# Kernel optimization log

Measured on AMD Instinct MI355X. Metric: run time of the kernel, lower is better.

The kernel has to match this reference:

```python
import jax, jax.numpy as jnp
import numpy as np
import math

N_HEADS = 16  # matches init_kwargs n_heads


def setup_inputs() -> dict:
    key = jax.random.key(0)
    k1, k2, k3 = jax.random.split(key, 3)
    B, S, D = 8, 1024, 1024
    x = jax.random.normal(k1, (B, S, D), dtype=jnp.float32)
    Wc = jax.random.normal(k2, (D, 3 * D), dtype=jnp.float32) * 0.02
    bc = jnp.zeros((3 * D,), dtype=jnp.float32)
    Wo = jax.random.normal(k3, (D, D), dtype=jnp.float32) * 0.02
    bo = jnp.zeros((D,), dtype=jnp.float32)
    return {"x": x, "Wc": Wc, "bc": bc, "Wo": Wo, "bo": bo}


def reference(x, Wc, bc, Wo, bo):
    B, S, D = x.shape
    H = N_HEADS
    hd = D // H
    qkv = x @ Wc + bc                         # [B,S,3D]
    q, k, v = jnp.split(qkv, 3, axis=2)
    q = q.reshape(B, S, H, hd)
    k = k.reshape(B, S, H, hd)
    v = v.reshape(B, S, H, hd)
    # NOTE: source scales by sqrt(d_size), not sqrt(head_dim)
    scores = jnp.einsum("bqhd,bkhd->bhqk", q, k) / math.sqrt(D)
    # source mask: triu(ones) kept, zeros (k < q) filled with float32 min
    # i.e. attend only to positions k >= q (anti-causal, faithful to source)
    keep = jnp.triu(jnp.ones((S, S), dtype=bool))  # [S,S]
    neg = jnp.finfo(jnp.float32).min
    scores = jnp.where(keep[None, None, :, :], scores, neg)
    attn = jax.nn.softmax(scores, axis=-1)    # [B,H,S,S]; dropout p=0 -> identity
    out = jnp.einsum("bhqk,bkhd->bqhd", attn, v)
    concat = out.reshape(B, S, D)
    return concat @ Wo + bo                   # final dropout p=0 -> identity
```

## Files before the change

### kernel.cpp

```cpp
#include <hip/hip_runtime.h>
#include <stdint.h>

typedef __attribute__((ext_vector_type(8))) short  bf16x8;
typedef __attribute__((ext_vector_type(4))) short  short4v;
typedef __attribute__((ext_vector_type(4))) float  f32x4;
typedef __attribute__((ext_vector_type(4))) float  float4v;

#define VMW(N) asm volatile("s_waitcnt vmcnt(" #N ")" ::: "memory")
#define BAR()  asm volatile("s_barrier" ::: "memory")

__device__ __forceinline__ short f2bf(float f) {
  union { float f; uint32_t u; } c; c.f = f;
  uint32_t u = c.u;
  uint32_t r = (u + 0x7FFFu + ((u >> 16) & 1u)) >> 16;
  return (short)(uint16_t)r;
}

__device__ __forceinline__ void gload_lds16(const void* g, void* l) {
  __builtin_amdgcn_global_load_lds(
      (const __attribute__((address_space(1))) void*)g,
      (__attribute__((address_space(3))) void*)l, 16, 0, 0);
}

__global__ __launch_bounds__(256) void k_f32_to_bf16(
    const float* __restrict__ in, short* __restrict__ out, int n4) {
  int i = blockIdx.x * 256 + threadIdx.x;
  if (i >= n4) return;
  float4v v = *(const float4v*)(in + (size_t)i * 4);
  short4v o;
  o.x = f2bf(v.x); o.y = f2bf(v.y); o.z = f2bf(v.z); o.w = f2bf(v.w);
  *(short4v*)(out + (size_t)i * 4) = o;
}

__global__ __launch_bounds__(256) void k_transpose_bf16(
    const float* __restrict__ in, short* __restrict__ out, int R, int C) {
  __shared__ short tile[64][65];
  int bc = blockIdx.x * 64, br = blockIdx.y * 64;
  int tc = threadIdx.x & 63, tr = threadIdx.x >> 6;
#pragma unroll
  for (int i = 0; i < 64; i += 4)
    tile[tc][tr + i] = f2bf(in[(size_t)(br + tr + i) * C + bc + tc]);
  __syncthreads();
#pragma unroll
  for (int i = 0; i < 64; i += 4)
    out[(size_t)(bc + tr + i) * R + br + tc] = tile[tr + i][tc];
}

template <bool F32OUT>
__global__ __launch_bounds__(256) void k_gemm2(
    const short* __restrict__ A, const short* __restrict__ BT,
    const float* __restrict__ bias, void* __restrict__ Cout,
    int M, int N, int K, int nbn) {
  __shared__ short SM[2][2][2][128][32];
  const int tid = threadIdx.x;
  const int w = tid >> 6, l = tid & 63;
  const int fr = l & 15, fg = l >> 4;
  const int wm = w >> 1, wn = w & 1;

  const int q8 = gridDim.x >> 3;
  const int wg = (blockIdx.x & 7) * q8 + (blockIdx.x >> 3);
  const int bm = wg / nbn, bn = wg % nbn;
  const size_t brow = (size_t)bm << 7;
  const int bcol = bn << 7;

  const int NT = K >> 6;

  const int srow = l >> 2;
  const int soct = (l & 3) ^ ((l >> 3) & 3);
  const short* aG = A + (brow + srow) * (size_t)K + soct * 8;
  const short* bG = BT + ((size_t)(bcol + srow)) * K + soct * 8;

  const int slot8 = ((fg ^ ((fr >> 1) & 3)) << 3);

  f32x4 acc[4][4] = {};

#pragma unroll
  for (int s = 0; s < 6; ++s) {
    const int t = s >> 2, tau = s & 3, buf = t & 1, mat = tau & 1, kh = tau >> 1;
    const int kbase = t * 64 + kh * 32;
    const short* g0 = (mat ? bG : aG) + kbase;
#pragma unroll
    for (int j = 0; j < 2; ++j) {
      const int r0 = (w * 2 + j) * 16;
      gload_lds16(g0 + (size_t)r0 * K, (char*)&SM[buf][mat][kh][r0][0]);
    }
  }
  VMW(8);
  BAR();

  int sidx = 6;
  for (int t = 0; t < NT; ++t) {
    const int buf = t & 1;
#pragma unroll
    for (int p = 0; p < 2; ++p) {
      const int kh = p;
#pragma unroll
      for (int s = 0; s < 2; ++s) {
        if (sidx < NT * 4) {
          const int ts = sidx >> 2, tau = sidx & 3;
          const int sb = ts & 1, mat = tau & 1, skh = tau >> 1;
          const int kbase = ts * 64 + skh * 32;
          const short* g0 = (mat ? bG : aG) + kbase;
#pragma unroll
          for (int j = 0; j < 2; ++j) {
            const int r0 = (w * 2 + j) * 16;
            gload_lds16(g0 + (size_t)r0 * K, (char*)&SM[sb][mat][skh][r0][0]);
          }
          ++sidx;
        }
      }
      bf16x8 af[4], bf[4];
#pragma unroll
      for (int m = 0; m < 4; ++m)
        af[m] = *(const bf16x8*)&SM[buf][0][kh][wm * 64 + m * 16 + fr][slot8];
#pragma unroll
      for (int n = 0; n < 4; ++n)
        bf[n] = *(const bf16x8*)&SM[buf][1][kh][wn * 64 + n * 16 + fr][slot8];
      BAR();
      __builtin_amdgcn_s_setprio(1);
#pragma unroll
      for (int m = 0; m < 4; ++m)
#pragma unroll
        for (int n = 0; n < 4; ++n)
          acc[m][n] = __builtin_amdgcn_mfma_f32_16x16x32_bf16(
              af[m], bf[n], acc[m][n], 0, 0, 0);
      __builtin_amdgcn_s_setprio(0);
      if (!(t == NT - 1 && p == 1)) {
        if (t == NT - 1 && p == 0) { VMW(0); }
        else if (t == NT - 2 && p == 1) { VMW(4); }
        else { VMW(8); }
        BAR();
      }
    }
  }

#pragma unroll
  for (int n = 0; n < 4; ++n) {
    const int col = bcol + wn * 64 + n * 16 + fr;
    const float bv = bias[col];
#pragma unroll
    for (int i = 0; i < 4; ++i) {
      const size_t row = brow + (size_t)(wm * 64 + i * 16 + fg * 4);
#pragma unroll
      for (int r = 0; r < 4; ++r) {
        const float v = acc[i][n][r] + bv;
        if (F32OUT)
          ((float*)Cout)[(row + r) * (size_t)N + col] = v;
        else
          ((short*)Cout)[(row + r) * (size_t)N + col] = f2bf(v);
      }
    }
  }
}

__global__ __launch_bounds__(256) void k_attn(
    const short* __restrict__ qkv, short* __restrict__ outc, int Bn, int S) {
  __shared__ short Ks[128][64];
  __shared__ short Vt[64][136];

  const int tid = threadIdx.x;
  const int w = tid >> 6, l = tid & 63;
  const int fr = l & 15, fg = l >> 4;

  const int tq = blockIdx.x >> 7;
  const int bh = blockIdx.x & 127;
  const int h = bh & 15, b = bh >> 4;
  const int q0 = tq << 6;

  const size_t rowbase = (size_t)b * S;
  const int qcol = q0 + w * 16 + fr;

  bf16x8 qf[2];
  {
    const short* qp = qkv + (rowbase + qcol) * 3072 + h * 64 + fg * 8;
    qf[0] = *(const bf16x8*)qp;
    qf[1] = *(const bf16x8*)(qp + 32);
  }

  f32x4 o[4] = {};
  float m2 = -3.0e38f, ls = 0.0f;

  const short* Kbase = qkv + rowbase * 3072 + 1024 + h * 64;
  const short* Vbase = qkv + rowbase * 3072 + 2048 + h * 64;
  const float C2 = 0.04508422f;

  const int c0 = tq >> 1;
  for (int c = c0; c < 8; ++c) {
    const int k0 = c << 7;
    {
      int r8 = l >> 3, slot = l & 7;
#pragma unroll
      for (int j = 0; j < 4; ++j) {
        int ch = w * 4 + j;
        int row = ch * 8 + r8;
        int d = (slot ^ (row & 7)) << 3;
        gload_lds16(Kbase + (size_t)(k0 + row) * 3072 + d,
                    (char*)&Ks[0][0] + ch * 1024);
      }
    }
    {
      int db = (tid >> 4) << 2;
#pragma unroll
      for (int kh = 0; kh < 2; ++kh) {
        int kb = ((tid & 15) << 2) + (kh << 6);
        const short* vp = Vbase + (size_t)(k0 + kb) * 3072 + db;
        short4v r0 = *(const short4v*)(vp);
        short4v r1 = *(const short4v*)(vp + 3072);
        short4v r2 = *(const short4v*)(vp + 2 * 3072);
        short4v r3 = *(const short4v*)(vp + 3 * 3072);
        short4v t0 = {r0.x, r1.x, r2.x, r3.x};
        short4v t1 = {r0.y, r1.y, r2.y, r3.y};
        short4v t2 = {r0.z, r1.z, r2.z, r3.z};
        short4v t3 = {r0.w, r1.w, r2.w, r3.w};
        *(short4v*)&Vt[db + 0][kb] = t0;
        *(short4v*)&Vt[db + 1][kb] = t1;
        *(short4v*)&Vt[db + 2][kb] = t2;
        *(short4v*)&Vt[db + 3][kb] = t3;
      }
    }
    __syncthreads();

    f32x4 st[8];
#pragma unroll
    for (int kb = 0; kb < 8; ++kb) {
      f32x4 z = {0.f, 0.f, 0.f, 0.f};
      int row = kb * 16 + fr;
      int sw = row & 7;
      bf16x8 kf0 = *(const bf16x8*)&Ks[row][(fg ^ sw) << 3];
      bf16x8 kf1 = *(const bf16x8*)&Ks[row][((4 + fg) ^ sw) << 3];
      z = __builtin_amdgcn_mfma_f32_16x16x32_bf16(kf0, qf[0], z, 0, 0, 0);
      z = __builtin_amdgcn_mfma_f32_16x16x32_bf16(kf1, qf[1], z, 0, 0, 0);
      st[kb] = z;
    }

    const bool masked = (c == c0);
    float pm = -3.0e38f;
#pragma unroll
    for (int kb = 0; kb < 8; ++kb)
#pragma unroll
      for (int r = 0; r < 4; ++r) {
        float s = st[kb][r] * C2;
        if (masked) {
          int kg = k0 + kb * 16 + fg * 4 + r;
          s = (kg < qcol) ? -3.0e38f : s;
        }
        st[kb][r] = s;
        pm = fmaxf(pm, s);
      }
    pm = fmaxf(pm, __shfl_xor(pm, 16, 64));
    pm = fmaxf(pm, __shfl_xor(pm, 32, 64));

    bool skip = __all(pm - m2 <= 8.0f);
    float mnew = skip ? m2 : fmaxf(m2, pm);
    float psum = 0.f;
#pragma unroll
    for (int kb = 0; kb < 8; ++kb)
#pragma unroll
      for (int r = 0; r < 4; ++r) {
        float e = exp2f(st[kb][r] - mnew);
        st[kb][r] = e;
        psum += e;
      }
    psum += __shfl_xor(psum, 16, 64);
    psum += __shfl_xor(psum, 32, 64);
    if (skip) {
      ls += psum;
    } else {
      float scl = exp2f(m2 - mnew);
      ls = ls * scl + psum;
      m2 = mnew;
#pragma unroll
      for (int r = 0; r < 4; ++r) {
        float so = __shfl(scl, fg * 4 + r, 64);
#pragma unroll
        for (int f = 0; f < 4; ++f) o[f][r] *= so;
      }
    }

#pragma unroll
    for (int kb2 = 0; kb2 < 4; ++kb2) {
      bf16x8 pa = {f2bf(st[2 * kb2][0]),     f2bf(st[2 * kb2][1]),
                   f2bf(st[2 * kb2][2]),     f2bf(st[2 * kb2][3]),
                   f2bf(st[2 * kb2 + 1][0]), f2bf(st[2 * kb2 + 1][1]),
                   f2bf(st[2 * kb2 + 1][2]), f2bf(st[2 * kb2 + 1][3])};
#pragma unroll
      for (int f = 0; f < 4; ++f) {
        short4v v0 = *(const short4v*)&Vt[f * 16 + fr][kb2 * 32 + fg * 4];
        short4v v1 = *(const short4v*)&Vt[f * 16 + fr][kb2 * 32 + 16 + fg * 4];
        bf16x8 vb = {v0.x, v0.y, v0.z, v0.w, v1.x, v1.y, v1.z, v1.w};
        o[f] = __builtin_amdgcn_mfma_f32_16x16x32_bf16(pa, vb, o[f], 0, 0, 0);
      }
    }
    __syncthreads();
  }

#pragma unroll
  for (int r = 0; r < 4; ++r) {
    float denom = __shfl(ls, fg * 4 + r, 64);
    float inv = 1.0f / denom;
    size_t orow = rowbase + (size_t)(q0 + w * 16 + fg * 4 + r);
    short* op = outc + orow * 1024 + h * 64 + fr;
#pragma unroll
    for (int f = 0; f < 4; ++f) op[f * 16] = f2bf(o[f][r] * inv);
  }
}

extern "C" void kernel_launch(void* const* d_in, const int* in_sizes, int n_in,
                              void* d_out, int out_size, void* d_ws,
                              size_t ws_size, hipStream_t stream) {
  const float* x = (const float*)d_in[0];
  const float* Wc = (const float*)d_in[1];
  const float* bc = (const float*)d_in[2];
  const float* Wo = (const float*)d_in[3];
  const float* bo = (const float*)d_in[4];
  float* out = (float*)d_out;

  const int Bn = 8, S = 1024, D = 1024;
  const int M = Bn * S;

  char* ws = (char*)d_ws;
  short* xb  = (short*)(ws);
  short* wct = (short*)(ws + (size_t)16 * 1024 * 1024);
  short* wot = (short*)(ws + (size_t)22 * 1024 * 1024);
  short* qkv = (short*)(ws + (size_t)24 * 1024 * 1024);
  short* cat = (short*)(ws + (size_t)72 * 1024 * 1024);

  k_f32_to_bf16<<<(M * D / 4 + 255) / 256, 256, 0, stream>>>(x, xb, M * D / 4);
  {
    dim3 g(3 * D / 64, D / 64);
    k_transpose_bf16<<<g, 256, 0, stream>>>(Wc, wct, D, 3 * D);
  }
  {
    dim3 g(D / 64, D / 64);
    k_transpose_bf16<<<g, 256, 0, stream>>>(Wo, wot, D, D);
  }
  k_gemm2<false><<<(M / 128) * (3 * D / 128), 256, 0, stream>>>(
      xb, wct, bc, qkv, M, 3 * D, D, 3 * D / 128);
  k_attn<<<16 * 128, 256, 0, stream>>>(qkv, cat, Bn, S);
  k_gemm2<true><<<(M / 128) * (D / 128), 256, 0, stream>>>(
      cat, wot, bo, out, M, D, D, D / 128);
}
```

Before: 172.6 us.

## Double-buffer K tiles and register-prefetch V in attention loop

The attention kernel now keeps two K tiles in LDS and issues the next chunk's K (via global_load_lds) and V (into registers) before computing the current chunk. The V transpose is written into LDS from the prefetched registers at the start of each iteration. The aim is to hide global memory latency behind the QK^T and softmax work. In exchange it uses more LDS and registers, which can lower occupancy. It also relies on raw s_barrier/vmcnt waits instead of __syncthreads, so LDS write visibility depends on the compiler inserting the needed waits.

```diff
diff --git a/kernel.cpp b/kernel.cpp
--- a/kernel.cpp
+++ b/kernel.cpp
@@ -69,7 +69,6 @@
   const int soct = (l & 3) ^ ((l >> 3) & 3);
   const short* aG = A + (brow + srow) * (size_t)K + soct * 8;
   const short* bG = BT + ((size_t)(bcol + srow)) * K + soct * 8;
-
   const int slot8 = ((fg ^ ((fr >> 1) & 3)) << 3);
 
   f32x4 acc[4][4] = {};
@@ -155,7 +154,7 @@
 
 __global__ __launch_bounds__(256) void k_attn(
     const short* __restrict__ qkv, short* __restrict__ outc, int Bn, int S) {
-  __shared__ short Ks[128][64];
+  __shared__ short Ks[2][128][64];
   __shared__ short Vt[64][136];
 
   const int tid = threadIdx.x;
@@ -184,41 +183,60 @@
   const short* Vbase = qkv + rowbase * 3072 + 2048 + h * 64;
   const float C2 = 0.04508422f;
 
+  const int r8 = l >> 3, slot = l & 7;
+  const int vdb = (tid >> 4) << 2;
+
+#define STAGE_K(c, bufv)                                                       \
+  {                                                                            \
+    const int k0s = (c) << 7;                                                  \
+    _Pragma("unroll") for (int j = 0; j < 4; ++j) {                            \
+      int ch = w * 4 + j;                                                      \
+      int row = ch * 8 + r8;                                                   \
+      int d = (slot ^ (row & 7)) << 3;                                         \
+      gload_lds16(Kbase + (size_t)(k0s + row) * 3072 + d,                      \
+                  (char*)&Ks[bufv][0][0] + ch * 1024);                         \
+    }                                                                          \
+  }
+#define LOAD_V(c, vr)                                                          \
+  {                                                                            \
+    const int k0s = (c) << 7;                                                  \
+    _Pragma("unroll") for (int kh = 0; kh < 2; ++kh) {                         \
+      int kb = ((tid & 15) << 2) + (kh << 6);                                  \
+      const short* vp = Vbase + (size_t)(k0s + kb) * 3072 + vdb;               \
+      vr[kh][0] = *(const short4v*)(vp);                                       \
+      vr[kh][1] = *(const short4v*)(vp + 3072);                                \
+      vr[kh][2] = *(const short4v*)(vp + 2 * 3072);                            \
+      vr[kh][3] = *(const short4v*)(vp + 3 * 3072);                            \
+    }                                                                          \
+  }
+
   const int c0 = tq >> 1;
+  short4v vr[2][4];
+  STAGE_K(c0, 0);
+  LOAD_V(c0, vr);
+  int cur = 0;
+
   for (int c = c0; c < 8; ++c) {
     const int k0 = c << 7;
-    {
-      int r8 = l >> 3, slot = l & 7;
-#pragma unroll
-      for (int j = 0; j < 4; ++j) {
-        int ch = w * 4 + j;
-        int row = ch * 8 + r8;
-        int d = (slot ^ (row & 7)) << 3;
-        gload_lds16(Kbase + (size_t)(k0 + row) * 3072 + d,
-                    (char*)&Ks[0][0] + ch * 1024);
-      }
-    }
-    {
-      int db = (tid >> 4) << 2;
-#pragma unroll
-      for (int kh = 0; kh < 2; ++kh) {
-        int kb = ((tid & 15) << 2) + (kh << 6);
-        const short* vp = Vbase + (size_t)(k0 + kb) * 3072 + db;
-        short4v r0 = *(const short4v*)(vp);
-        short4v r1 = *(const short4v*)(vp + 3072);
-        short4v r2 = *(const short4v*)(vp + 2 * 3072);
-        short4v r3 = *(const short4v*)(vp + 3 * 3072);
-        short4v t0 = {r0.x, r1.x, r2.x, r3.x};
-        short4v t1 = {r0.y, r1.y, r2.y, r3.y};
-        short4v t2 = {r0.z, r1.z, r2.z, r3.z};
-        short4v t3 = {r0.w, r1.w, r2.w, r3.w};
-        *(short4v*)&Vt[db + 0][kb] = t0;
-        *(short4v*)&Vt[db + 1][kb] = t1;
-        *(short4v*)&Vt[db + 2][kb] = t2;
-        *(short4v*)&Vt[db + 3][kb] = t3;
-      }
-    }
-    __syncthreads();
+    VMW(0);
+    BAR();
+
+#pragma unroll
+    for (int kh = 0; kh < 2; ++kh) {
+      int kb = ((tid & 15) << 2) + (kh << 6);
+      short4v t0 = {vr[kh][0].x, vr[kh][1].x, vr[kh][2].x, vr[kh][3].x};
+      short4v t1 = {vr[kh][0].y, vr[kh][1].y, vr[kh][2].y, vr[kh][3].y};
+      short4v t2 = {vr[kh][0].z, vr[kh][1].z, vr[kh][2].z, vr[kh][3].z};
+      short4v t3 = {vr[kh][0].w, vr[kh][1].w, vr[kh][2].w, vr[kh][3].w};
+      *(short4v*)&Vt[vdb + 0][kb] = t0;
+      *(short4v*)&Vt[vdb + 1][kb] = t1;
+      *(short4v*)&Vt[vdb + 2][kb] = t2;
+      *(short4v*)&Vt[vdb + 3][kb] = t3;
+    }
+    if (c + 1 < 8) {
+      STAGE_K(c + 1, cur ^ 1);
+      LOAD_V(c + 1, vr);
+    }
 
     f32x4 st[8];
 #pragma unroll
@@ -226,8 +244,8 @@
       f32x4 z = {0.f, 0.f, 0.f, 0.f};
       int row = kb * 16 + fr;
       int sw = row & 7;
-      bf16x8 kf0 = *(const bf16x8*)&Ks[row][(fg ^ sw) << 3];
-      bf16x8 kf1 = *(const bf16x8*)&Ks[row][((4 + fg) ^ sw) << 3];
+      bf16x8 kf0 = *(const bf16x8*)&Ks[cur][row][(fg ^ sw) << 3];
+      bf16x8 kf1 = *(const bf16x8*)&Ks[cur][row][((4 + fg) ^ sw) << 3];
       z = __builtin_amdgcn_mfma_f32_16x16x32_bf16(kf0, qf[0], z, 0, 0, 0);
       z = __builtin_amdgcn_mfma_f32_16x16x32_bf16(kf1, qf[1], z, 0, 0, 0);
       st[kb] = z;
@@ -277,6 +295,8 @@
       }
     }
 
+    BAR();
+
 #pragma unroll
     for (int kb2 = 0; kb2 < 4; ++kb2) {
       bf16x8 pa = {f2bf(st[2 * kb2][0]),     f2bf(st[2 * kb2][1]),
@@ -291,8 +311,10 @@
         o[f] = __builtin_amdgcn_mfma_f32_16x16x32_bf16(pa, vb, o[f], 0, 0, 0);
       }
     }
-    __syncthreads();
-  }
+    cur ^= 1;
+  }
+#undef STAGE_K
+#undef LOAD_V
 
 #pragma unroll
   for (int r = 0; r < 4; ++r) {
```

Result: slower. 176.2 us (+2.1%).
